# Kernel tuning notes

Hardware: AMD Instinct MI355X
Metric: run time of the kernel (lower is better)

Reference implementation:

```python
import jax, jax.numpy as jnp
import numpy as np

D_MODEL = 2048; N_LAYERS = 2; ED = 4096; D_STATE = 16; D_CONV = 4; DT_RANK = 128
N_HEADS = 4; HEAD_DIM = D_MODEL // N_HEADS
B = 4; L = 256


def setup_inputs() -> dict:
    key = jax.random.key(0)
    ks = jax.random.split(key, 12)
    def nrm(k, shape, s=0.02):
        return jax.random.normal(k, shape, jnp.float32) * s
    p = {}
    p["x"] = jax.random.normal(ks[0], (B, L, D_MODEL), jnp.float32)
    p["norm_w"] = jnp.ones((N_LAYERS, D_MODEL), jnp.float32)
    p["in_proj_w"] = nrm(ks[1], (N_LAYERS, 2 * ED, D_MODEL))
    p["conv_w"] = nrm(ks[2], (N_LAYERS, ED, 1, D_CONV), 0.2)
    p["conv_b"] = jnp.zeros((N_LAYERS, ED), jnp.float32)
    p["x_proj_w"] = nrm(ks[3], (N_LAYERS, DT_RANK + 2 * D_STATE, ED))
    p["dt_proj_w"] = nrm(ks[4], (N_LAYERS, ED, DT_RANK), 0.05)
    p["dt_proj_b"] = nrm(ks[5], (N_LAYERS, ED), 0.1) - 4.0  # small positive deltas after softplus
    p["A_log"] = jnp.tile(jnp.log(jnp.arange(1, D_STATE + 1, dtype=jnp.float32)), (N_LAYERS, ED, 1))
    p["D_param"] = jnp.ones((N_LAYERS, ED), jnp.float32)
    p["out_proj_w"] = nrm(ks[6], (N_LAYERS, D_MODEL, ED))
    p["attn_in_w"] = nrm(ks[7], (3 * D_MODEL, D_MODEL))
    p["attn_in_b"] = jnp.zeros((3 * D_MODEL,), jnp.float32)
    p["attn_out_w"] = nrm(ks[8], (D_MODEL, D_MODEL))
    p["attn_out_b"] = jnp.zeros((D_MODEL,), jnp.float32)
    p["w1"] = nrm(ks[9], (1024, D_MODEL)); p["b1"] = jnp.zeros((1024,), jnp.float32)
    p["ln_g"] = jnp.ones((1024,), jnp.float32); p["ln_b"] = jnp.zeros((1024,), jnp.float32)
    p["w2"] = nrm(ks[10], (64, 1024)); p["b2"] = jnp.zeros((64,), jnp.float32)
    return p


def _rmsnorm(x, w, eps=1e-5):
    return x * jax.lax.rsqrt(jnp.mean(x * x, axis=-1, keepdims=True) + eps) * w


def _mamba_block(x, in_w, cw, cb, xp_w, dt_w, dt_b, A_log, Dp, out_w):
    b = x.shape[0]
    xz = jnp.einsum('bld,ed->ble', x, in_w)  # (B,L,2*ED)
    xin, z = jnp.split(xz, 2, axis=-1)
    # depthwise causal conv1d (torch pads d_conv-1 both sides then truncates to L == left-pad only)
    xc = jax.lax.conv_general_dilated(
        xin.transpose(0, 2, 1), cw, (1,), [(D_CONV - 1, 0)],
        dimension_numbers=('NCH', 'OIH', 'NCH'), feature_group_count=ED)
    xc = (xc + cb[None, :, None]).transpose(0, 2, 1)  # (B,L,ED)
    xc = jax.nn.silu(xc)
    dbc = jnp.einsum('ble,re->blr', xc, xp_w)
    dt, Bm, Cm = jnp.split(dbc, [DT_RANK, DT_RANK + D_STATE], axis=-1)
    delta = jax.nn.softplus(jnp.einsum('blr,er->ble', dt, dt_w) + dt_b)  # (B,L,ED)
    A = -jnp.exp(A_log)  # (ED,N)
    dA = jnp.exp(delta[..., None] * A)                         # (B,L,ED,N)
    dBx = delta[..., None] * Bm[:, :, None, :] * xc[..., None]  # (B,L,ED,N)
    def step(h, inp):
        a, bb = inp
        h = a * h + bb
        return h, h
    h0 = jnp.zeros((b, ED, D_STATE), x.dtype)
    _, hs = jax.lax.scan(step, h0, (jnp.moveaxis(dA, 1, 0), jnp.moveaxis(dBx, 1, 0)))
    y = jnp.einsum('lbdn,bln->bld', hs, Cm) + xc * Dp
    y = y * jax.nn.silu(z)
    return jnp.einsum('ble,de->bld', y, out_w)


def reference(x, norm_w, in_proj_w, conv_w, conv_b, x_proj_w, dt_proj_w, dt_proj_b,
              A_log, D_param, out_proj_w, attn_in_w, attn_in_b, attn_out_w, attn_out_b,
              w1, b1, ln_g, ln_b, w2, b2):
    h = x
    for i in range(N_LAYERS):  # residual Mamba blocks
        h = h + _mamba_block(_rmsnorm(h, norm_w[i]), in_proj_w[i], conv_w[i], conv_b[i],
                             x_proj_w[i], dt_proj_w[i], dt_proj_b[i], A_log[i],
                             D_param[i], out_proj_w[i])
    seq = h
    # nn.MultiheadAttention (batch_first, eval -> no dropout)
    qkv = jnp.einsum('bld,ed->ble', seq, attn_in_w) + attn_in_b
    q, k, v = jnp.split(qkv, 3, axis=-1)
    def heads(t):
        return t.reshape(t.shape[0], t.shape[1], N_HEADS, HEAD_DIM)
    q, k, v = heads(q), heads(k), heads(v)
    scores = jnp.einsum('bqhd,bkhd->bhqk', q, k) / np.float32(np.sqrt(HEAD_DIM))
    attn = jax.nn.softmax(scores, axis=-1)
    ao = jnp.einsum('bhqk,bkhd->bqhd', attn, v).reshape(seq.shape)
    ao = jnp.einsum('bld,ed->ble', ao, attn_out_w) + attn_out_b
    o = ao + seq
    last = o[:, -1, :]  # (B, D_MODEL)
    hm = jnp.einsum('bd,hd->bh', last, w1) + b1
    mu = jnp.mean(hm, axis=-1, keepdims=True)
    var = jnp.mean((hm - mu) ** 2, axis=-1, keepdims=True)
    hm = (hm - mu) * jax.lax.rsqrt(var + 1e-5) * ln_g + ln_b
    hm = jax.nn.elu(hm)
    outv = jnp.einsum('bh,oh->bo', hm, w2) + b2
    n2 = jnp.sqrt(jnp.sum(outv * outv, axis=-1, keepdims=True))
    return outv / jnp.maximum(n2, 1e-12)
```

## Files before the change

### kernel.cpp

```cpp
#include <hip/hip_runtime.h>
#include <hip/hip_bf16.h>
#include <math.h>

#define D_MODEL 2048
#define N_LAYERS 2
#define ED 4096
#define D_STATE 16
#define D_CONV 4
#define DT_RANK 128
#define N_HEADS 4
#define HEAD_DIM 512
#define BATCH 4
#define SEQL 256

typedef __bf16 bf16_t;
typedef bf16_t bf16x8 __attribute__((ext_vector_type(8)));
typedef bf16_t bf16x4 __attribute__((ext_vector_type(4)));
typedef float f32x4 __attribute__((ext_vector_type(4)));

__device__ __forceinline__ float warp_reduce_sum(float v) {
#pragma unroll
    for (int off = 1; off < 64; off <<= 1) v += __shfl_xor(v, off);
    return v;
}
__device__ __forceinline__ float warp_reduce_max(float v) {
#pragma unroll
    for (int off = 1; off < 64; off <<= 1) v = fmaxf(v, __shfl_xor(v, off));
    return v;
}

__device__ __forceinline__ void gload_lds16(const bf16_t* g, bf16_t* l) {
    __builtin_amdgcn_global_load_lds(
        (const __attribute__((address_space(1))) unsigned int*)g,
        (__attribute__((address_space(3))) unsigned int*)l, 16, 0, 0);
}

__global__ void copy_kernel(const float* __restrict__ src, float* __restrict__ dst, int n) {
    int i = blockIdx.x * blockDim.x + threadIdx.x;
    if (i < n) dst[i] = src[i];
}

__global__ void f2b_kernel(const float* __restrict__ src, bf16_t* __restrict__ dst, int n) {
    int i = blockIdx.x * blockDim.x + threadIdx.x;
    if (i < n) dst[i] = (bf16_t)src[i];
}

__global__ void f2b8_kernel(const float* __restrict__ src, bf16_t* __restrict__ dst, long n8) {
    long i = (long)blockIdx.x * blockDim.x + threadIdx.x;
    if (i >= n8) return;
    float4 a = ((const float4*)src)[2 * i];
    float4 b = ((const float4*)src)[2 * i + 1];
    bf16x8 o;
    o[0] = (bf16_t)a.x; o[1] = (bf16_t)a.y; o[2] = (bf16_t)a.z; o[3] = (bf16_t)a.w;
    o[4] = (bf16_t)b.x; o[5] = (bf16_t)b.y; o[6] = (bf16_t)b.z; o[7] = (bf16_t)b.w;
    ((bf16x8*)dst)[i] = o;
}

__global__ void dt_pack_kernel(const float* __restrict__ dbc, bf16_t* __restrict__ dt) {
    int i = blockIdx.x * blockDim.x + threadIdx.x;
    int row = i >> 7, col = i & 127;
    dt[i] = (bf16_t)dbc[row * (DT_RANK + 2 * D_STATE) + col];
}

__global__ void ksum_kernel(const float* __restrict__ part, float* __restrict__ out, int n,
                            int nz, long stride) {
    int i = blockIdx.x * blockDim.x + threadIdx.x;
    if (i >= n) return;
    float s = 0.f;
    for (int z = 0; z < nz; ++z) s += part[(long)z * stride + i];
    out[i] = s;
}

__global__ void ksum_add_kernel(const float* __restrict__ part, float* __restrict__ out, int n,
                                int nz, long stride, const float* __restrict__ bias, int bmask) {
    int i = blockIdx.x * blockDim.x + threadIdx.x;
    if (i >= n) return;
    float s = out[i];
    for (int z = 0; z < nz; ++z) s += part[(long)z * stride + i];
    if (bias) s += bias[i & bmask];
    out[i] = s;
}

__global__ void rmsnorm_kernel(const float* __restrict__ x, const float* __restrict__ w,
                               bf16_t* __restrict__ o) {
    int row = blockIdx.x;
    int tid = threadIdx.x;
    const float* xr = x + (long)row * D_MODEL;
    float ss = 0.f;
    for (int i = tid; i < D_MODEL; i += 256) { float v = xr[i]; ss += v * v; }
    ss = warp_reduce_sum(ss);
    __shared__ float r[4];
    int wave = tid >> 6;
    if ((tid & 63) == 0) r[wave] = ss;
    __syncthreads();
    float tot = r[0] + r[1] + r[2] + r[3];
    float sc = rsqrtf(tot / (float)D_MODEL + 1e-5f);
    bf16_t* orow = o + (long)row * D_MODEL;
    for (int i = tid; i < D_MODEL; i += 256) orow[i] = (bf16_t)(xr[i] * sc * w[i]);
}

__global__ __launch_bounds__(256, 2) void gemm_bf16(
    const bf16_t* __restrict__ A, int lda, const float* __restrict__ B, int ldb,
    float* __restrict__ C, int ldc, int N, int K_len, const float* __restrict__ bias,
    int accumulate, int out_bf16, long partial_stride) {
    __shared__ bf16_t As[128 * 32];
    __shared__ bf16_t Bs[128 * 32];
    const int tid = threadIdx.x;
    const int lane = tid & 63;
    const int wave = tid >> 6;
    const int m0 = blockIdx.y * 128;
    const int n0 = blockIdx.x * 128;
    const int kbeg = blockIdx.z * K_len;

    const int cA = wave * 2;
    const bf16_t* gA0 = A + (long)(m0 + cA * 16 + (lane >> 2)) * lda + kbeg + (lane & 3) * 8;
    const bf16_t* gA1 = gA0 + 16L * lda;
    bf16_t* lA0 = &As[cA * 512];
    bf16_t* lA1 = &As[cA * 512 + 512];

    const int brow = tid >> 1;
    const int bcol = (tid & 1) * 16;
    const bool bvalid = (n0 + brow) < N;
    const float* gB = B + (long)(n0 + brow) * ldb + kbeg + bcol;
    bf16_t* lB = &Bs[brow * 32 + bcol];

    const int wr = wave >> 1, wc = wave & 1;
    const int fr = lane & 15, fq = lane >> 4;
    const bf16_t* aBase = &As[(wr * 64 + fr) * 32 + fq * 8];
    const bf16_t* bBase = &Bs[(wc * 64 + fr) * 32 + fq * 8];

    f32x4 acc[4][4] = {};

    for (int kk = 0; kk < K_len; kk += 32) {
        gload_lds16(gA0, lA0);
        gload_lds16(gA1, lA1);
        gA0 += 32;
        gA1 += 32;
        if (bvalid) {
            float4 v0 = *(const float4*)(gB);
            float4 v1 = *(const float4*)(gB + 4);
            float4 v2 = *(const float4*)(gB + 8);
            float4 v3 = *(const float4*)(gB + 12);
            gB += 32;
            bf16x8 p0, p1;
            p0[0] = (bf16_t)v0.x; p0[1] = (bf16_t)v0.y; p0[2] = (bf16_t)v0.z; p0[3] = (bf16_t)v0.w;
            p0[4] = (bf16_t)v1.x; p0[5] = (bf16_t)v1.y; p0[6] = (bf16_t)v1.z; p0[7] = (bf16_t)v1.w;
            p1[0] = (bf16_t)v2.x; p1[1] = (bf16_t)v2.y; p1[2] = (bf16_t)v2.z; p1[3] = (bf16_t)v2.w;
            p1[4] = (bf16_t)v3.x; p1[5] = (bf16_t)v3.y; p1[6] = (bf16_t)v3.z; p1[7] = (bf16_t)v3.w;
            *(bf16x8*)lB = p0;
            *((bf16x8*)lB + 1) = p1;
        }
        __syncthreads();
        bf16x8 af[4], bfr[4];
#pragma unroll
        for (int m = 0; m < 4; ++m) af[m] = *(const bf16x8*)(aBase + m * 512);
#pragma unroll
        for (int n = 0; n < 4; ++n) bfr[n] = *(const bf16x8*)(bBase + n * 512);
#pragma unroll
        for (int m = 0; m < 4; ++m)
#pragma unroll
            for (int n = 0; n < 4; ++n)
                acc[m][n] = __builtin_amdgcn_mfma_f32_16x16x32_bf16(af[m], bfr[n], acc[m][n], 0, 0, 0);
        __syncthreads();
    }

    float* Cz = C + ((gridDim.z > 1) ? (long)blockIdx.z * partial_stride : 0L);
#pragma unroll
    for (int m = 0; m < 4; ++m) {
        const int grow0 = m0 + wr * 64 + m * 16 + fq * 4;
#pragma unroll
        for (int n = 0; n < 4; ++n) {
            const int gcol = n0 + wc * 64 + n * 16 + fr;
            if (gcol >= N) continue;
            float bv = bias ? bias[gcol] : 0.f;
#pragma unroll
            for (int r = 0; r < 4; ++r) {
                long idx = (long)(grow0 + r) * ldc + gcol;
                float v = acc[m][n][r] + bv;
                if (out_bf16) {
                    ((bf16_t*)Cz)[idx] = (bf16_t)v;
                } else {
                    if (accumulate) v += Cz[idx];
                    Cz[idx] = v;
                }
            }
        }
    }
}

__global__ __launch_bounds__(256, 4) void gemm_w64(
    const bf16_t* __restrict__ A, int lda, const bf16_t* __restrict__ B, int ldb,
    void* __restrict__ Cv, int ldc, int K_len, const float* __restrict__ bias,
    int out_bf16, long partial_stride) {
    __shared__ bf16_t As[64 * 32];
    __shared__ bf16_t Bs[128 * 32];
    const int tid = threadIdx.x;
    const int lane = tid & 63;
    const int wave = tid >> 6;
    const int m0 = blockIdx.y * 64;
    const int n0 = blockIdx.x * 128;
    const int kbeg = blockIdx.z * K_len;

    const bf16_t* gA = A + (long)(m0 + wave * 16 + (lane >> 2)) * lda + kbeg + (lane & 3) * 8;
    bf16_t* lA = &As[wave * 512];
    const bf16_t* gB0 = B + (long)(n0 + wave * 32 + (lane >> 2)) * ldb + kbeg + (lane & 3) * 8;
    const bf16_t* gB1 = gB0 + 16L * ldb;
    bf16_t* lB0 = &Bs[wave * 1024];
    bf16_t* lB1 = lB0 + 512;

    const int wr = wave >> 1, wc = wave & 1;
    const int fr = lane & 15, fq = lane >> 4;
    const bf16_t* aBase = &As[(wr * 32 + fr) * 32 + fq * 8];
    const bf16_t* bBase = &Bs[(wc * 64 + fr) * 32 + fq * 8];

    f32x4 acc[2][4] = {};

    for (int kk = 0; kk < K_len; kk += 32) {
        gload_lds16(gA, lA);
        gload_lds16(gB0, lB0);
        gload_lds16(gB1, lB1);
        gA += 32; gB0 += 32; gB1 += 32;
        __syncthreads();
        bf16x8 af[2], bfr[4];
#pragma unroll
        for (int m = 0; m < 2; ++m) af[m] = *(const bf16x8*)(aBase + m * 512);
#pragma unroll
        for (int n = 0; n < 4; ++n) bfr[n] = *(const bf16x8*)(bBase + n * 512);
#pragma unroll
        for (int m = 0; m < 2; ++m)
#pragma unroll
            for (int n = 0; n < 4; ++n)
                acc[m][n] = __builtin_amdgcn_mfma_f32_16x16x32_bf16(af[m], bfr[n], acc[m][n], 0, 0, 0);
        __syncthreads();
    }

    float* Cz = (float*)Cv + ((gridDim.z > 1) ? (long)blockIdx.z * partial_stride : 0L);
#pragma unroll
    for (int m = 0; m < 2; ++m) {
        const int grow0 = m0 + wr * 32 + m * 16 + fq * 4;
#pragma unroll
        for (int n = 0; n < 4; ++n) {
            const int gcol = n0 + wc * 64 + n * 16 + fr;
            float bv = bias ? bias[gcol] : 0.f;
#pragma unroll
            for (int r = 0; r < 4; ++r) {
                long idx = (long)(grow0 + r) * ldc + gcol;
                float v = acc[m][n][r] + bv;
                if (out_bf16) ((bf16_t*)Cv)[idx] = (bf16_t)v;
                else Cz[idx] = v;
            }
        }
    }
}

__global__ __launch_bounds__(256, 2) void gemm_bb(
    const bf16_t* __restrict__ A, long aO, long aI, int lda,
    const bf16_t* __restrict__ B, long bO, long bI, int ldb,
    void* __restrict__ Cv, long cO, long cI, int ldc,
    int K_len, int out_bf16) {
    __shared__ bf16_t As[128 * 32];
    __shared__ bf16_t Bs[128 * 32];
    const int tid = threadIdx.x;
    const int lane = tid & 63;
    const int wave = tid >> 6;
    const int z = blockIdx.z, zb = z >> 2, zh = z & 3;
    const bf16_t* Az = A + (long)zb * aO + (long)zh * aI;
    const bf16_t* Bz = B + (long)zb * bO + (long)zh * bI;
    const int m0 = blockIdx.y * 128;
    const int n0 = blockIdx.x * 128;

    const int cA = wave * 2;
    const bf16_t* gA0 = Az + (long)(m0 + cA * 16 + (lane >> 2)) * lda + (lane & 3) * 8;
    const bf16_t* gA1 = gA0 + 16L * lda;
    const bf16_t* gB0 = Bz + (long)(n0 + cA * 16 + (lane >> 2)) * ldb + (lane & 3) * 8;
    const bf16_t* gB1 = gB0 + 16L * ldb;
    bf16_t* lA0 = &As[cA * 512];
    bf16_t* lA1 = lA0 + 512;
    bf16_t* lB0 = &Bs[cA * 512];
    bf16_t* lB1 = lB0 + 512;

    const int wr = wave >> 1, wc = wave & 1;
    const int fr = lane & 15, fq = lane >> 4;
    const bf16_t* aBase = &As[(wr * 64 + fr) * 32 + fq * 8];
    const bf16_t* bBase = &Bs[(wc * 64 + fr) * 32 + fq * 8];

    f32x4 acc[4][4] = {};

    for (int kk = 0; kk < K_len; kk += 32) {
        gload_lds16(gA0, lA0);
        gload_lds16(gA1, lA1);
        gload_lds16(gB0, lB0);
        gload_lds16(gB1, lB1);
        gA0 += 32; gA1 += 32; gB0 += 32; gB1 += 32;
        __syncthreads();
        bf16x8 af[4], bfr[4];
#pragma unroll
        for (int m = 0; m < 4; ++m) af[m] = *(const bf16x8*)(aBase + m * 512);
#pragma unroll
        for (int n = 0; n < 4; ++n) bfr[n] = *(const bf16x8*)(bBase + n * 512);
#pragma unroll
        for (int m = 0; m < 4; ++m)
#pragma unroll
            for (int n = 0; n < 4; ++n)
                acc[m][n] = __builtin_amdgcn_mfma_f32_16x16x32_bf16(af[m], bfr[n], acc[m][n], 0, 0, 0);
        __syncthreads();
    }

#pragma unroll
    for (int m = 0; m < 4; ++m) {
        const int grow0 = m0 + wr * 64 + m * 16 + fq * 4;
#pragma unroll
        for (int n = 0; n < 4; ++n) {
            const int gcol = n0 + wc * 64 + n * 16 + fr;
#pragma unroll
            for (int r = 0; r < 4; ++r) {
                long idx = (long)(grow0 + r) * ldc + gcol;
                if (out_bf16) {
                    bf16_t* Cb = (bf16_t*)Cv + (long)zb * cO + (long)zh * cI;
                    Cb[idx] = (bf16_t)acc[m][n][r];
                } else {
                    float* Cf = (float*)Cv + (long)zb * cO + (long)zh * cI;
                    Cf[idx] = acc[m][n][r];
                }
            }
        }
    }
}

__global__ void vtrans_kernel(const bf16_t* __restrict__ qkvb, bf16_t* __restrict__ vt) {
    int z = blockIdx.z;
    int b = z >> 2, h = z & 3;
    int d0 = blockIdx.x * 64, k0 = blockIdx.y * 64;
    __shared__ bf16_t tile[64][72];
    int t = threadIdx.x;
    int r = t >> 2;
    int c4 = (t & 3) * 16;
    const bf16_t* src = qkvb + ((long)(b * SEQL + k0 + r)) * (3 * D_MODEL) + 2 * D_MODEL +
                        h * HEAD_DIM + d0 + c4;
    bf16x8 v0 = *(const bf16x8*)src;
    bf16x8 v1 = *(const bf16x8*)(src + 8);
#pragma unroll
    for (int j = 0; j < 8; ++j) tile[r][c4 + j] = v0[j];
#pragma unroll
    for (int j = 0; j < 8; ++j) tile[r][c4 + 8 + j] = v1[j];
    __syncthreads();
    int dd = t >> 2, kc = (t & 3) * 16;
    bf16_t* dst = vt + (long)z * (HEAD_DIM * SEQL) + (long)(d0 + dd) * SEQL + k0 + kc;
    bf16x8 o0, o1;
#pragma unroll
    for (int j = 0; j < 8; ++j) o0[j] = tile[kc + j][dd];
#pragma unroll
    for (int j = 0; j < 8; ++j) o1[j] = tile[kc + 8 + j][dd];
    *(bf16x8*)dst = o0;
    *(bf16x8*)(dst + 8) = o1;
}

__global__ void softmax_kernel(const float* __restrict__ S, bf16_t* __restrict__ P) {
    long row = blockIdx.x;
    int tid = threadIdx.x;
    float s = S[row * SEQL + tid] * 0.044194173824159216f;
    __shared__ float red[4];
    float m = warp_reduce_max(s);
    if ((tid & 63) == 0) red[tid >> 6] = m;
    __syncthreads();
    float gm = fmaxf(fmaxf(red[0], red[1]), fmaxf(red[2], red[3]));
    __syncthreads();
    float p = __expf(s - gm);
    float su = warp_reduce_sum(p);
    if ((tid & 63) == 0) red[tid >> 6] = su;
    __syncthreads();
    float gs = red[0] + red[1] + red[2] + red[3];
    P[row * SEQL + tid] = (bf16_t)(p / gs);
}

__global__ void conv_tr_kernel(const bf16_t* __restrict__ xzb, const float* __restrict__ cw,
                               const float* __restrict__ cb, bf16_t* __restrict__ xT,
                               bf16_t* __restrict__ xcb, bf16_t* __restrict__ zT) {
    __shared__ bf16_t xin[68][64];
    __shared__ bf16_t outt[64][72];
    const int e0 = blockIdx.x * 64, l0 = blockIdx.y * 64, b = blockIdx.z;
    const int t = threadIdx.x;
    const int r = t >> 4;
    const int c = (t & 15) * 4;

#pragma unroll
    for (int i = 0; i < 5; ++i) {
        int m = r + i * 16;
        if (m < 67) {
            int l = l0 - 3 + m;
            bf16x4 v;
            if (l >= 0)
                v = *(const bf16x4*)(xzb + ((long)(b * SEQL + l)) * (2 * ED) + e0 + c);
            else {
                v[0] = (bf16_t)0.f; v[1] = (bf16_t)0.f; v[2] = (bf16_t)0.f; v[3] = (bf16_t)0.f;
            }
            *(bf16x4*)&xin[m][c] = v;
        }
    }
    __syncthreads();

    {
        const int e_l = t & 63;
        const int lbase = (t >> 6) * 16;
        const float4 wv = *(const float4*)(cw + (long)(e0 + e_l) * 4);
        const float bias = cb[e0 + e_l];
#pragma unroll
        for (int k = 0; k < 16; ++k) {
            int l = lbase + k;
            float acc = bias + wv.x * (float)xin[l][e_l] + wv.y * (float)xin[l + 1][e_l] +
                        wv.z * (float)xin[l + 2][e_l] + wv.w * (float)xin[l + 3][e_l];
            float s = acc / (1.f + __expf(-acc));
            outt[e_l][l] = (bf16_t)s;
        }
    }
    __syncthreads();

    {
        int er = t >> 2, lc = (t & 3) * 16;
        bf16x8 a = *(bf16x8*)&outt[er][lc];
        bf16x8 bb8 = *(bf16x8*)&outt[er][lc + 8];
        bf16_t* dst = xT + ((long)b * ED + e0 + er) * SEQL + l0 + lc;
        *(bf16x8*)dst = a;
        *(bf16x8*)(dst + 8) = bb8;
    }
    {
        int lr = t >> 2, ec = (t & 3) * 16;
        bf16_t tmp[16];
#pragma unroll
        for (int j = 0; j < 16; ++j) tmp[j] = outt[ec + j][lr];
        bf16_t* dst = xcb + ((long)(b * SEQL + l0 + lr)) * ED + e0 + ec;
        *(bf16x8*)dst = *(bf16x8*)&tmp[0];
        *(bf16x8*)(dst + 8) = *(bf16x8*)&tmp[8];
    }
    __syncthreads();

#pragma unroll
    for (int i = 0; i < 4; ++i) {
        int m = r + i * 16;
        bf16x4 v = *(const bf16x4*)(xzb + ((long)(b * SEQL + l0 + m)) * (2 * ED) + ED + e0 + c);
        *(bf16x4*)&xin[m][c] = v;
    }
    __syncthreads();
    {
        int er = t >> 2, lc = (t & 3) * 16;
        bf16_t tz[16];
#pragma unroll
        for (int j = 0; j < 16; ++j) tz[j] = xin[lc + j][er];
        bf16_t* dst = zT + ((long)b * ED + e0 + er) * SEQL + l0 + lc;
        *(bf16x8*)dst = *(bf16x8*)&tz[0];
        *(bf16x8*)(dst + 8) = *(bf16x8*)&tz[8];
    }
}

__global__ void softplus_tr_kernel(const float* __restrict__ delta, const float* __restrict__ dt_b,
                                   float* __restrict__ dT) {
    __shared__ float tile[64][65];
    const int e0 = blockIdx.x * 64, l0 = blockIdx.y * 64, b = blockIdx.z;
    const int t = threadIdx.x;
    const int r = t >> 4, c = (t & 15) * 4;
#pragma unroll
    for (int i = 0; i < 4; ++i) {
        int l = r + i * 16;
        float4 v = *(const float4*)(delta + ((long)(b * SEQL + l0 + l)) * ED + e0 + c);
        float4 bb = *(const float4*)(dt_b + e0 + c);
        float u0 = v.x + bb.x, u1 = v.y + bb.y, u2 = v.z + bb.z, u3 = v.w + bb.w;
        tile[l][c] = (u0 > 20.f) ? u0 : log1pf(__expf(u0));
        tile[l][c + 1] = (u1 > 20.f) ? u1 : log1pf(__expf(u1));
        tile[l][c + 2] = (u2 > 20.f) ? u2 : log1pf(__expf(u2));
        tile[l][c + 3] = (u3 > 20.f) ? u3 : log1pf(__expf(u3));
    }
    __syncthreads();
#pragma unroll
    for (int i = 0; i < 4; ++i) {
        int ee = r + i * 16;
        float4 w;
        w.x = tile[c][ee];
        w.y = tile[c + 1][ee];
        w.z = tile[c + 2][ee];
        w.w = tile[c + 3][ee];
        *(float4*)(dT + ((long)b * ED + e0 + ee) * SEQL + l0 + c) = w;
    }
}

__global__ __launch_bounds__(256) void scan_chunk_kernel(
    const float* __restrict__ dT, const bf16_t* __restrict__ xT, const bf16_t* __restrict__ zT,
    const float* __restrict__ dbc, const float* __restrict__ A_log, const float* __restrict__ Dp,
    bf16_t* __restrict__ yT) {
    __shared__ float bc[SEQL][36];
    const int t = threadIdx.x;
    const int chunk = t & 15;
    const int el = t >> 4;
    const int b = blockIdx.y;
    const int e = blockIdx.x * 16 + el;
    const int l0 = chunk * 16;
    const int R = DT_RANK + 2 * D_STATE;

    {
        const int row0 = t >> 3;
        const int col = (t & 7) * 4;
        const float* src = dbc + (long)b * SEQL * R + DT_RANK;
#pragma unroll
        for (int it = 0; it < 8; ++it) {
            int row = row0 + it * 32;
            int prow = ((row & 15) << 4) | (row >> 4);
            *(float4*)&bc[prow][col] = *(const float4*)(src + (long)row * R + col);
        }
    }

    float Ar[16];
    {
        const float* ap = A_log + (long)e * D_STATE;
#pragma unroll
        for (int n = 0; n < 16; n += 4) {
            float4 v = *(const float4*)(ap + n);
            Ar[n] = -__expf(v.x);
            Ar[n + 1] = -__expf(v.y);
            Ar[n + 2] = -__expf(v.z);
            Ar[n + 3] = -__expf(v.w);
        }
    }
    float d[16];
    {
        const float* dp = dT + ((long)b * ED + e) * SEQL + l0;
#pragma unroll
        for (int j = 0; j < 16; j += 4) *(float4*)&d[j] = *(const float4*)(dp + j);
    }
    float xf[16];
    {
        const bf16_t* xp = xT + ((long)b * ED + e) * SEQL + l0;
        bf16x8 x0 = *(const bf16x8*)xp;
        bf16x8 x1 = *(const bf16x8*)(xp + 8);
#pragma unroll
        for (int j = 0; j < 8; ++j) {
            xf[j] = (float)x0[j];
            xf[8 + j] = (float)x1[j];
        }
    }
    __syncthreads();

    float P[16], S[16];
#pragma unroll
    for (int n = 0; n < 16; ++n) {
        P[n] = 1.f;
        S[n] = 0.f;
    }

#pragma unroll
    for (int j = 0; j < 16; ++j) {
        const float* br = &bc[(j << 4) | chunk][0];
        float dj = d[j];
        float dx = dj * xf[j];
#pragma unroll
        for (int n = 0; n < 16; ++n) {
            float dA = __expf(dj * Ar[n]);
            S[n] = dA * S[n] + dx * br[n];
            P[n] *= dA;
        }
    }

#pragma unroll
    for (int off = 1; off < 16; off <<= 1) {
        float Pp[16], Sp[16];
#pragma unroll
        for (int n = 0; n < 16; ++n) {
            Pp[n] = __shfl_up(P[n], off, 16);
            Sp[n] = __shfl_up(S[n], off, 16);
        }
        if (chunk >= off) {
#pragma unroll
            for (int n = 0; n < 16; ++n) {
                S[n] = P[n] * Sp[n] + S[n];
                P[n] *= Pp[n];
            }
        }
    }

    float h[16];
#pragma unroll
    for (int n = 0; n < 16; ++n) {
        float hs = __shfl_up(S[n], 1, 16);
        h[n] = (chunk == 0) ? 0.f : hs;
    }

    const float dpe = Dp[e];
    float yf[16];
#pragma unroll
    for (int j = 0; j < 16; ++j) {
        const float* br = &bc[(j << 4) | chunk][0];
        float dj = d[j];
        float dx = dj * xf[j];
        float y = 0.f;
#pragma unroll
        for (int n = 0; n < 16; ++n) {
            float dA = __expf(dj * Ar[n]);
            h[n] = dA * h[n] + dx * br[n];
            y += h[n] * br[16 + n];
        }
        yf[j] = y + xf[j] * dpe;
    }

    const bf16_t* zp = zT + ((long)b * ED + e) * SEQL + l0;
    bf16_t* yp = yT + ((long)b * ED + e) * SEQL + l0;
    {
        bf16x8 z0 = *(const bf16x8*)zp;
        bf16x8 o0;
#pragma unroll
        for (int j = 0; j < 8; ++j) {
            float z = (float)z0[j];
            o0[j] = (bf16_t)(yf[j] * (z / (1.f + __expf(-z))));
        }
        *(bf16x8*)yp = o0;
        bf16x8 z1 = *(const bf16x8*)(zp + 8);
        bf16x8 o1;
#pragma unroll
        for (int j = 0; j < 8; ++j) {
            float z = (float)z1[j];
            o1[j] = (bf16_t)(yf[8 + j] * (z / (1.f + __expf(-z))));
        }
        *(bf16x8*)(yp + 8) = o1;
    }
}

__global__ void ytr_kernel(const bf16_t* __restrict__ yT, bf16_t* __restrict__ Y) {
    __shared__ bf16_t tl[64][72];
    const int e0 = blockIdx.x * 64, l0 = blockIdx.y * 64, b = blockIdx.z;
    const int t = threadIdx.x;
    {
        int er = t >> 2, lc = (t & 3) * 16;
        const bf16_t* src = yT + ((long)b * ED + e0 + er) * SEQL + l0 + lc;
        bf16x8 a = *(const bf16x8*)src;
        bf16x8 bb8 = *(const bf16x8*)(src + 8);
        *(bf16x8*)&tl[er][lc] = a;
        *(bf16x8*)&tl[er][lc + 8] = bb8;
    }
    __syncthreads();
    {
        int lr = t >> 2, ec = (t & 3) * 16;
        bf16_t tmp[16];
#pragma unroll
        for (int j = 0; j < 16; ++j) tmp[j] = tl[ec + j][lr];
        bf16_t* dst = Y + ((long)(b * SEQL + l0 + lr)) * ED + e0 + ec;
        *(bf16x8*)dst = *(bf16x8*)&tmp[0];
        *(bf16x8*)(dst + 8) = *(bf16x8*)&tmp[8];
    }
}

__global__ void head_gemv1(const float* __restrict__ H, const float* __restrict__ w1,
                           const float* __restrict__ b1, float* __restrict__ hm1) {
    int b = blockIdx.y;
    int wave = threadIdx.x >> 6, lane = threadIdx.x & 63;
    int n = blockIdx.x * 4 + wave;
    const float* last = H + ((long)(b * SEQL + SEQL - 1)) * D_MODEL;
    const float* wr = w1 + (long)n * D_MODEL;
    float s = 0.f;
    for (int j = lane * 4; j < D_MODEL; j += 256) {
        float4 a = *(const float4*)(last + j);
        float4 w = *(const float4*)(wr + j);
        s += a.x * w.x + a.y * w.y + a.z * w.z + a.w * w.w;
    }
    s = warp_reduce_sum(s);
    if (lane == 0) hm1[b * 1024 + n] = s + b1[n];
}

__global__ void head_final(const float* __restrict__ hm1, const float* __restrict__ ln_g,
                           const float* __restrict__ ln_b, const float* __restrict__ w2,
                           const float* __restrict__ b2, float* __restrict__ out) {
    int b = blockIdx.x;
    int tid = threadIdx.x;
    __shared__ float hm[1024];
    __shared__ float r1[16], r2[16];
    __shared__ float stats[2];
    __shared__ float outs[64];

    float v = hm1[b * 1024 + tid];
    float s1 = warp_reduce_sum(v);
    float s2 = warp_reduce_sum(v * v);
    int wave = tid >> 6;
    if ((tid & 63) == 0) { r1[wave] = s1; r2[wave] = s2; }
    __syncthreads();
    if (tid == 0) {
        float t1 = 0.f, t2 = 0.f;
        for (int w = 0; w < 16; ++w) { t1 += r1[w]; t2 += r2[w]; }
        float mean = t1 / 1024.f;
        stats[0] = mean;
        stats[1] = rsqrtf(t2 / 1024.f - mean * mean + 1e-5f);
    }
    __syncthreads();
    float x = (v - stats[0]) * stats[1] * ln_g[tid] + ln_b[tid];
    x = (x > 0.f) ? x : (__expf(x) - 1.f);
    hm[tid] = x;
    __syncthreads();

    int o = tid >> 4, kk = tid & 15;
    float a = 0.f;
    const float* w2r = w2 + (long)o * 1024;
    for (int j = kk; j < 1024; j += 16) a += hm[j] * w2r[j];
#pragma unroll
    for (int off = 1; off < 16; off <<= 1) a += __shfl_xor(a, off);
    if (kk == 0) outs[o] = a + b2[o];
    __syncthreads();
    if (tid < 64) {
        float vv = outs[tid];
        float ss = warp_reduce_sum(vv * vv);
        out[b * 64 + tid] = vv / fmaxf(sqrtf(ss), 1e-12f);
    }
}

extern "C" void kernel_launch(void* const* d_in, const int* in_sizes, int n_in,
                              void* d_out, int out_size, void* d_ws, size_t ws_size,
                              hipStream_t stream) {
    const float* x = (const float*)d_in[0];
    const float* norm_w = (const float*)d_in[1];
    const float* in_proj_w = (const float*)d_in[2];
    const float* conv_w = (const float*)d_in[3];
    const float* conv_b = (const float*)d_in[4];
    const float* x_proj_w = (const float*)d_in[5];
    const float* dt_proj_w = (const float*)d_in[6];
    const float* dt_proj_b = (const float*)d_in[7];
    const float* A_log = (const float*)d_in[8];
    const float* D_param = (const float*)d_in[9];
    const float* out_proj_w = (const float*)d_in[10];
    const float* attn_in_w = (const float*)d_in[11];
    const float* attn_in_b = (const float*)d_in[12];
    const float* attn_out_w = (const float*)d_in[13];
    const float* attn_out_b = (const float*)d_in[14];
    const float* w1 = (const float*)d_in[15];
    const float* b1 = (const float*)d_in[16];
    const float* ln_g = (const float*)d_in[17];
    const float* ln_b = (const float*)d_in[18];
    const float* w2 = (const float*)d_in[19];
    const float* b2 = (const float*)d_in[20];

    float* ws = (float*)d_ws;
    float* H = ws;
    float* SCR = ws + 2097152;
    bf16_t* XNb = (bf16_t*)(ws + 8388608);
    float* DELTA = ws + 9437184;
    float* DBC = ws + 13631488;
    float* XPART = ws + 13795328;
    bf16_t* XCb = (bf16_t*)(ws + 15106048);
    bf16_t* DTb = (bf16_t*)(ws + 17203200);
    bf16_t* Yb = (bf16_t*)(ws + 17268736);
    bf16_t* Hb = (bf16_t*)(ws + 19365888);
    bf16_t* AOb = (bf16_t*)(ws + 20414464);
    float* HM1 = ws + 21463040;
    bf16_t* XT = (bf16_t*)(ws + 21467136);
    bf16_t* ZT = (bf16_t*)(ws + 23564288);

    bf16_t* WBin = (bf16_t*)(ws + 9437184);
    bf16_t* WBout = (bf16_t*)(ws + 21467136);
    bf16_t* WBai = (bf16_t*)(ws + 8388608);
    bf16_t* WBao = (bf16_t*)(ws + 21467136);

    bf16_t* XZb = (bf16_t*)SCR;
    float* DTT = SCR;
    bf16_t* YTT = (bf16_t*)(SCR + 4194304);
    float* PART = SCR;

    bf16_t* QKVb = (bf16_t*)SCR;
    float* SBUF = SCR + 3145728;
    bf16_t* Pb = (bf16_t*)(SCR + 3145728 + 1048576);
    bf16_t* VTb = (bf16_t*)(SCR + 3145728 + 1048576 + 524288);

    const int M = BATCH * SEQL;
    const long S_H = (long)M * D_MODEL;

    copy_kernel<<<(S_H + 255) / 256, 256, 0, stream>>>(x, H, (int)S_H);

    for (int i = 0; i < N_LAYERS; ++i) {
        rmsnorm_kernel<<<M, 256, 0, stream>>>(H, norm_w + (long)i * D_MODEL, XNb);
        f2b8_kernel<<<8192, 256, 0, stream>>>(in_proj_w + (long)i * 2 * ED * D_MODEL, WBin,
                                              (long)2 * ED * D_MODEL / 8);
        gemm_w64<<<dim3(64, 16, 1), 256, 0, stream>>>(XNb, D_MODEL, WBin, D_MODEL, XZb, 2 * ED,
                                                      D_MODEL, nullptr, 1, 0);
        conv_tr_kernel<<<dim3(64, 4, 4), 256, 0, stream>>>(
            XZb, conv_w + (long)i * ED * D_CONV, conv_b + (long)i * ED, XT, XCb, ZT);
        gemm_bf16<<<dim3(2, 8, 8), 256, 0, stream>>>(
            XCb, ED, x_proj_w + (long)i * (DT_RANK + 2 * D_STATE) * ED, ED, XPART,
            DT_RANK + 2 * D_STATE, DT_RANK + 2 * D_STATE, ED / 8, nullptr, 0, 0,
            (long)M * (DT_RANK + 2 * D_STATE));
        ksum_kernel<<<640, 256, 0, stream>>>(XPART, DBC, M * (DT_RANK + 2 * D_STATE), 8,
                                             (long)M * (DT_RANK + 2 * D_STATE));
        dt_pack_kernel<<<512, 256, 0, stream>>>(DBC, DTb);
        gemm_bf16<<<dim3(32, 8, 1), 256, 0, stream>>>(
            DTb, DT_RANK, dt_proj_w + (long)i * ED * DT_RANK, DT_RANK, DELTA, ED, ED, DT_RANK,
            nullptr, 0, 0, 0);
        softplus_tr_kernel<<<dim3(64, 4, 4), 256, 0, stream>>>(DELTA, dt_proj_b + (long)i * ED,
                                                               DTT);
        scan_chunk_kernel<<<dim3(ED / 16, BATCH), 256, 0, stream>>>(
            DTT, XT, ZT, DBC, A_log + (long)i * ED * D_STATE, D_param + (long)i * ED, YTT);
        ytr_kernel<<<dim3(64, 4, 4), 256, 0, stream>>>(YTT, Yb);
        f2b8_kernel<<<4096, 256, 0, stream>>>(out_proj_w + (long)i * D_MODEL * ED, WBout,
                                              (long)D_MODEL * ED / 8);
        gemm_w64<<<dim3(16, 16, 4), 256, 0, stream>>>(Yb, ED, WBout, ED, PART, D_MODEL, ED / 4,
                                                      nullptr, 0, (long)M * D_MODEL);
        ksum_add_kernel<<<8192, 256, 0, stream>>>(PART, H, M * D_MODEL, 4, (long)M * D_MODEL,
                                                  nullptr, 0);
    }

    f2b_kernel<<<(int)((S_H + 255) / 256), 256, 0, stream>>>(H, Hb, (int)S_H);
    f2b8_kernel<<<6144, 256, 0, stream>>>(attn_in_w, WBai, (long)3 * D_MODEL * D_MODEL / 8);
    gemm_w64<<<dim3(48, 16, 1), 256, 0, stream>>>(Hb, D_MODEL, WBai, D_MODEL, QKVb, 3 * D_MODEL,
                                                  D_MODEL, attn_in_b, 1, 0);
    vtrans_kernel<<<dim3(8, 4, 16), 256, 0, stream>>>(QKVb, VTb);
    gemm_bb<<<dim3(2, 2, 16), 256, 0, stream>>>(
        QKVb, (long)SEQL * 3 * D_MODEL, HEAD_DIM, 3 * D_MODEL,
        QKVb + D_MODEL, (long)SEQL * 3 * D_MODEL, HEAD_DIM, 3 * D_MODEL,
        SBUF, 4L * SEQL * SEQL, (long)SEQL * SEQL, SEQL, HEAD_DIM, 0);
    softmax_kernel<<<BATCH * N_HEADS * SEQL, 256, 0, stream>>>(SBUF, Pb);
    gemm_bb<<<dim3(4, 2, 16), 256, 0, stream>>>(
        Pb, 4L * SEQL * SEQL, (long)SEQL * SEQL, SEQL,
        VTb, 4L * HEAD_DIM * SEQL, (long)HEAD_DIM * SEQL, SEQL,
        AOb, (long)SEQL * D_MODEL, HEAD_DIM, D_MODEL, SEQL, 1);
    f2b8_kernel<<<2048, 256, 0, stream>>>(attn_out_w, WBao, (long)D_MODEL * D_MODEL / 8);
    gemm_w64<<<dim3(16, 16, 4), 256, 0, stream>>>(AOb, D_MODEL, WBao, D_MODEL, PART, D_MODEL,
                                                  D_MODEL / 4, nullptr, 0, (long)M * D_MODEL);
    ksum_add_kernel<<<8192, 256, 0, stream>>>(PART, H, M * D_MODEL, 4, (long)M * D_MODEL,
                                              attn_out_b, D_MODEL - 1);

    head_gemv1<<<dim3(256, 4), 256, 0, stream>>>(H, w1, b1, HM1);
    head_final<<<BATCH, 1024, 0, stream>>>(HM1, ln_g, ln_b, w2, b2, (float*)d_out);
}
```

Measured before the change: 677.3 us.

## Fuse softplus/transposes into dt GEMM epilogue, vectorize copies, shrink attention GEMM tiles

```diff
diff --git a/kernel.cpp b/kernel.cpp
--- a/kernel.cpp
+++ b/kernel.cpp
@@ -35,14 +35,9 @@
         (__attribute__((address_space(3))) unsigned int*)l, 16, 0, 0);
 }
 
-__global__ void copy_kernel(const float* __restrict__ src, float* __restrict__ dst, int n) {
+__global__ void copy4_kernel(const float4* __restrict__ src, float4* __restrict__ dst, int n4) {
     int i = blockIdx.x * blockDim.x + threadIdx.x;
-    if (i < n) dst[i] = src[i];
-}
-
-__global__ void f2b_kernel(const float* __restrict__ src, bf16_t* __restrict__ dst, int n) {
-    int i = blockIdx.x * blockDim.x + threadIdx.x;
-    if (i < n) dst[i] = (bf16_t)src[i];
+    if (i < n4) dst[i] = src[i];
 }
 
 __global__ void f2b8_kernel(const float* __restrict__ src, bf16_t* __restrict__ dst, long n8) {
@@ -56,19 +51,16 @@
     ((bf16x8*)dst)[i] = o;
 }
 
-__global__ void dt_pack_kernel(const float* __restrict__ dbc, bf16_t* __restrict__ dt) {
-    int i = blockIdx.x * blockDim.x + threadIdx.x;
-    int row = i >> 7, col = i & 127;
-    dt[i] = (bf16_t)dbc[row * (DT_RANK + 2 * D_STATE) + col];
-}
-
-__global__ void ksum_kernel(const float* __restrict__ part, float* __restrict__ out, int n,
-                            int nz, long stride) {
+__global__ void ksum_dt_kernel(const float* __restrict__ part, float* __restrict__ out,
+                               bf16_t* __restrict__ dtb, int n, int nz, long stride) {
     int i = blockIdx.x * blockDim.x + threadIdx.x;
     if (i >= n) return;
     float s = 0.f;
     for (int z = 0; z < nz; ++z) s += part[(long)z * stride + i];
     out[i] = s;
+    int row = i / 160;
+    int col = i - row * 160;
+    if (col < DT_RANK) dtb[row * DT_RANK + col] = (bf16_t)s;
 }
 
 __global__ void ksum_add_kernel(const float* __restrict__ part, float* __restrict__ out, int n,
@@ -102,7 +94,7 @@
 __global__ __launch_bounds__(256, 2) void gemm_bf16(
     const bf16_t* __restrict__ A, int lda, const float* __restrict__ B, int ldb,
     float* __restrict__ C, int ldc, int N, int K_len, const float* __restrict__ bias,
-    int accumulate, int out_bf16, long partial_stride) {
+    int out_mode, long partial_stride) {
     __shared__ bf16_t As[128 * 32];
     __shared__ bf16_t Bs[128 * 32];
     const int tid = threadIdx.x;
@@ -164,6 +156,28 @@
         __syncthreads();
     }
 
+    if (out_mode == 2) {
+#pragma unroll
+        for (int m = 0; m < 4; ++m) {
+            const int grow0 = m0 + wr * 64 + m * 16 + fq * 4;
+            const int bb = grow0 >> 8;
+            const int l = grow0 & 255;
+#pragma unroll
+            for (int n = 0; n < 4; ++n) {
+                const int gcol = n0 + wc * 64 + n * 16 + fr;
+                const float bv = bias[gcol];
+                float4 w;
+                float u;
+                u = acc[m][n][0] + bv; w.x = (u > 20.f) ? u : log1pf(__expf(u));
+                u = acc[m][n][1] + bv; w.y = (u > 20.f) ? u : log1pf(__expf(u));
+                u = acc[m][n][2] + bv; w.z = (u > 20.f) ? u : log1pf(__expf(u));
+                u = acc[m][n][3] + bv; w.w = (u > 20.f) ? u : log1pf(__expf(u));
+                *(float4*)(C + ((long)bb * ED + gcol) * SEQL + l) = w;
+            }
+        }
+        return;
+    }
+
     float* Cz = C + ((gridDim.z > 1) ? (long)blockIdx.z * partial_stride : 0L);
 #pragma unroll
     for (int m = 0; m < 4; ++m) {
@@ -176,13 +190,7 @@
 #pragma unroll
             for (int r = 0; r < 4; ++r) {
                 long idx = (long)(grow0 + r) * ldc + gcol;
-                float v = acc[m][n][r] + bv;
-                if (out_bf16) {
-                    ((bf16_t*)Cz)[idx] = (bf16_t)v;
-                } else {
-                    if (accumulate) v += Cz[idx];
-                    Cz[idx] = v;
-                }
+                Cz[idx] = acc[m][n][r] + bv;
             }
         }
     }
@@ -253,12 +261,12 @@
     }
 }
 
-__global__ __launch_bounds__(256, 2) void gemm_bb(
+__global__ __launch_bounds__(256, 4) void gemm_bb64(
     const bf16_t* __restrict__ A, long aO, long aI, int lda,
     const bf16_t* __restrict__ B, long bO, long bI, int ldb,
     void* __restrict__ Cv, long cO, long cI, int ldc,
     int K_len, int out_bf16) {
-    __shared__ bf16_t As[128 * 32];
+    __shared__ bf16_t As[64 * 32];
     __shared__ bf16_t Bs[128 * 32];
     const int tid = threadIdx.x;
     const int lane = tid & 63;
@@ -266,40 +274,36 @@
     const int z = blockIdx.z, zb = z >> 2, zh = z & 3;
     const bf16_t* Az = A + (long)zb * aO + (long)zh * aI;
     const bf16_t* Bz = B + (long)zb * bO + (long)zh * bI;
-    const int m0 = blockIdx.y * 128;
+    const int m0 = blockIdx.y * 64;
     const int n0 = blockIdx.x * 128;
 
-    const int cA = wave * 2;
-    const bf16_t* gA0 = Az + (long)(m0 + cA * 16 + (lane >> 2)) * lda + (lane & 3) * 8;
-    const bf16_t* gA1 = gA0 + 16L * lda;
-    const bf16_t* gB0 = Bz + (long)(n0 + cA * 16 + (lane >> 2)) * ldb + (lane & 3) * 8;
+    const bf16_t* gA = Az + (long)(m0 + wave * 16 + (lane >> 2)) * lda + (lane & 3) * 8;
+    bf16_t* lA = &As[wave * 512];
+    const bf16_t* gB0 = Bz + (long)(n0 + wave * 32 + (lane >> 2)) * ldb + (lane & 3) * 8;
     const bf16_t* gB1 = gB0 + 16L * ldb;
-    bf16_t* lA0 = &As[cA * 512];
-    bf16_t* lA1 = lA0 + 512;
-    bf16_t* lB0 = &Bs[cA * 512];
+    bf16_t* lB0 = &Bs[wave * 1024];
     bf16_t* lB1 = lB0 + 512;
 
     const int wr = wave >> 1, wc = wave & 1;
     const int fr = lane & 15, fq = lane >> 4;
-    const bf16_t* aBase = &As[(wr * 64 + fr) * 32 + fq * 8];
+    const bf16_t* aBase = &As[(wr * 32 + fr) * 32 + fq * 8];
     const bf16_t* bBase = &Bs[(wc * 64 + fr) * 32 + fq * 8];
 
-    f32x4 acc[4][4] = {};
+    f32x4 acc[2][4] = {};
 
     for (int kk = 0; kk < K_len; kk += 32) {
-        gload_lds16(gA0, lA0);
-        gload_lds16(gA1, lA1);
+        gload_lds16(gA, lA);
         gload_lds16(gB0, lB0);
         gload_lds16(gB1, lB1);
-        gA0 += 32; gA1 += 32; gB0 += 32; gB1 += 32;
+        gA += 32; gB0 += 32; gB1 += 32;
         __syncthreads();
-        bf16x8 af[4], bfr[4];
-#pragma unroll
-        for (int m = 0; m < 4; ++m) af[m] = *(const bf16x8*)(aBase + m * 512);
+        bf16x8 af[2], bfr[4];
+#pragma unroll
+        for (int m = 0; m < 2; ++m) af[m] = *(const bf16x8*)(aBase + m * 512);
 #pragma unroll
         for (int n = 0; n < 4; ++n) bfr[n] = *(const bf16x8*)(bBase + n * 512);
 #pragma unroll
-        for (int m = 0; m < 4; ++m)
+        for (int m = 0; m < 2; ++m)
 #pragma unroll
             for (int n = 0; n < 4; ++n)
                 acc[m][n] = __builtin_amdgcn_mfma_f32_16x16x32_bf16(af[m], bfr[n], acc[m][n], 0, 0, 0);
@@ -307,8 +311,8 @@
     }
 
 #pragma unroll
-    for (int m = 0; m < 4; ++m) {
-        const int grow0 = m0 + wr * 64 + m * 16 + fq * 4;
+    for (int m = 0; m < 2; ++m) {
+        const int grow0 = m0 + wr * 32 + m * 16 + fq * 4;
 #pragma unroll
         for (int n = 0; n < 4; ++n) {
             const int gcol = n0 + wc * 64 + n * 16 + fr;
@@ -449,36 +453,6 @@
         bf16_t* dst = zT + ((long)b * ED + e0 + er) * SEQL + l0 + lc;
         *(bf16x8*)dst = *(bf16x8*)&tz[0];
         *(bf16x8*)(dst + 8) = *(bf16x8*)&tz[8];
-    }
-}
-
-__global__ void softplus_tr_kernel(const float* __restrict__ delta, const float* __restrict__ dt_b,
-                                   float* __restrict__ dT) {
-    __shared__ float tile[64][65];
-    const int e0 = blockIdx.x * 64, l0 = blockIdx.y * 64, b = blockIdx.z;
-    const int t = threadIdx.x;
-    const int r = t >> 4, c = (t & 15) * 4;
-#pragma unroll
-    for (int i = 0; i < 4; ++i) {
-        int l = r + i * 16;
-        float4 v = *(const float4*)(delta + ((long)(b * SEQL + l0 + l)) * ED + e0 + c);
-        float4 bb = *(const float4*)(dt_b + e0 + c);
-        float u0 = v.x + bb.x, u1 = v.y + bb.y, u2 = v.z + bb.z, u3 = v.w + bb.w;
-        tile[l][c] = (u0 > 20.f) ? u0 : log1pf(__expf(u0));
-        tile[l][c + 1] = (u1 > 20.f) ? u1 : log1pf(__expf(u1));
-        tile[l][c + 2] = (u2 > 20.f) ? u2 : log1pf(__expf(u2));
-        tile[l][c + 3] = (u3 > 20.f) ? u3 : log1pf(__expf(u3));
-    }
-    __syncthreads();
-#pragma unroll
-    for (int i = 0; i < 4; ++i) {
-        int ee = r + i * 16;
-        float4 w;
-        w.x = tile[c][ee];
-        w.y = tile[c + 1][ee];
-        w.z = tile[c + 2][ee];
-        w.w = tile[c + 3][ee];
-        *(float4*)(dT + ((long)b * ED + e0 + ee) * SEQL + l0 + c) = w;
     }
 }
 
@@ -735,7 +709,7 @@
     float* H = ws;
     float* SCR = ws + 2097152;
     bf16_t* XNb = (bf16_t*)(ws + 8388608);
-    float* DELTA = ws + 9437184;
+    float* DELTA_unused = ws + 9437184;
     float* DBC = ws + 13631488;
     float* XPART = ws + 13795328;
     bf16_t* XCb = (bf16_t*)(ws + 15106048);
@@ -746,6 +720,7 @@
     float* HM1 = ws + 21463040;
     bf16_t* XT = (bf16_t*)(ws + 21467136);
     bf16_t* ZT = (bf16_t*)(ws + 23564288);
+    (void)DELTA_unused;
 
     bf16_t* WBin = (bf16_t*)(ws + 9437184);
     bf16_t* WBout = (bf16_t*)(ws + 21467136);
@@ -765,7 +740,7 @@
     const int M = BATCH * SEQL;
     const long S_H = (long)M * D_MODEL;
 
-    copy_kernel<<<(S_H + 255) / 256, 256, 0, stream>>>(x, H, (int)S_H);
+    copy4_kernel<<<2048, 256, 0, stream>>>((const float4*)x, (float4*)H, (int)(S_H / 4));
 
     for (int i = 0; i < N_LAYERS; ++i) {
         rmsnorm_kernel<<<M, 256, 0, stream>>>(H, norm_w + (long)i * D_MODEL, XNb);
@@ -777,16 +752,13 @@
             XZb, conv_w + (long)i * ED * D_CONV, conv_b + (long)i * ED, XT, XCb, ZT);
         gemm_bf16<<<dim3(2, 8, 8), 256, 0, stream>>>(
             XCb, ED, x_proj_w + (long)i * (DT_RANK + 2 * D_STATE) * ED, ED, XPART,
-            DT_RANK + 2 * D_STATE, DT_RANK + 2 * D_STATE, ED / 8, nullptr, 0, 0,
+            DT_RANK + 2 * D_STATE, DT_RANK + 2 * D_STATE, ED / 8, nullptr, 0,
             (long)M * (DT_RANK + 2 * D_STATE));
-        ksum_kernel<<<640, 256, 0, stream>>>(XPART, DBC, M * (DT_RANK + 2 * D_STATE), 8,
-                                             (long)M * (DT_RANK + 2 * D_STATE));
-        dt_pack_kernel<<<512, 256, 0, stream>>>(DBC, DTb);
+        ksum_dt_kernel<<<640, 256, 0, stream>>>(XPART, DBC, DTb, M * (DT_RANK + 2 * D_STATE), 8,
+                                                (long)M * (DT_RANK + 2 * D_STATE));
         gemm_bf16<<<dim3(32, 8, 1), 256, 0, stream>>>(
-            DTb, DT_RANK, dt_proj_w + (long)i * ED * DT_RANK, DT_RANK, DELTA, ED, ED, DT_RANK,
-            nullptr, 0, 0, 0);
-        softplus_tr_kernel<<<dim3(64, 4, 4), 256, 0, stream>>>(DELTA, dt_proj_b + (long)i * ED,
-                                                               DTT);
+            DTb, DT_RANK, dt_proj_w + (long)i * ED * DT_RANK, DT_RANK, DTT, 0, ED, DT_RANK,
+            dt_proj_b + (long)i * ED, 2, 0);
         scan_chunk_kernel<<<dim3(ED / 16, BATCH), 256, 0, stream>>>(
             DTT, XT, ZT, DBC, A_log + (long)i * ED * D_STATE, D_param + (long)i * ED, YTT);
         ytr_kernel<<<dim3(64, 4, 4), 256, 0, stream>>>(YTT, Yb);
@@ -798,17 +770,17 @@
                                                   nullptr, 0);
     }
 
-    f2b_kernel<<<(int)((S_H + 255) / 256), 256, 0, stream>>>(H, Hb, (int)S_H);
+    f2b8_kernel<<<1024, 256, 0, stream>>>(H, Hb, S_H / 8);
     f2b8_kernel<<<6144, 256, 0, stream>>>(attn_in_w, WBai, (long)3 * D_MODEL * D_MODEL / 8);
     gemm_w64<<<dim3(48, 16, 1), 256, 0, stream>>>(Hb, D_MODEL, WBai, D_MODEL, QKVb, 3 * D_MODEL,
                                                   D_MODEL, attn_in_b, 1, 0);
     vtrans_kernel<<<dim3(8, 4, 16), 256, 0, stream>>>(QKVb, VTb);
-    gemm_bb<<<dim3(2, 2, 16), 256, 0, stream>>>(
+    gemm_bb64<<<dim3(2, 4, 16), 256, 0, stream>>>(
         QKVb, (long)SEQL * 3 * D_MODEL, HEAD_DIM, 3 * D_MODEL,
         QKVb + D_MODEL, (long)SEQL * 3 * D_MODEL, HEAD_DIM, 3 * D_MODEL,
         SBUF, 4L * SEQL * SEQL, (long)SEQL * SEQL, SEQL, HEAD_DIM, 0);
     softmax_kernel<<<BATCH * N_HEADS * SEQL, 256, 0, stream>>>(SBUF, Pb);
-    gemm_bb<<<dim3(4, 2, 16), 256, 0, stream>>>(
+    gemm_bb64<<<dim3(4, 4, 16), 256, 0, stream>>>(
         Pb, 4L * SEQL * SEQL, (long)SEQL * SEQL, SEQL,
         VTb, 4L * HEAD_DIM * SEQL, (long)HEAD_DIM * SEQL, SEQL,
         AOb, (long)SEQL * D_MODEL, HEAD_DIM, D_MODEL, SEQL, 1);
```

Measured after the change: 662.5 us. 2.2% less time.
